# Kernel optimization log

Hardware: AMD Instinct MI355X
Metric: run time of the kernel (lower is better)

## Reference

```python
import jax, jax.numpy as jnp
import numpy as np

N, IN_FEATURES, OUT_FEATURES = 131072, 128, 512


def setup_inputs() -> dict:
    key = jax.random.key(0)
    k1, k2 = jax.random.split(key)
    x = jax.random.normal(k1, (N, IN_FEATURES), dtype=jnp.float32)
    centers = jax.random.normal(k2, (OUT_FEATURES, IN_FEATURES), dtype=jnp.float32)  # nn.init.normal_(0,1)
    log_sigmas = jnp.zeros((OUT_FEATURES,), dtype=jnp.float32)  # nn.init.constant_(0)
    return {"x": x, "centers": centers, "log_sigmas": log_sigmas}


def reference(x, centers, log_sigmas):
    # (N, out, in) expanded intermediate of the torch code; same math).
    x_sq = jnp.sum(x * x, axis=-1, keepdims=True)            # (N, 1)
    c_sq = jnp.sum(centers * centers, axis=-1)               # (out,)
    cross = x @ centers.T                                    # (N, out) GEMM
    d2 = jnp.maximum(x_sq - 2.0 * cross + c_sq[None, :], 0.0)
    distances = jnp.sqrt(d2) / jnp.exp(log_sigmas)[None, :]  # (N, out)
    # gaussian basis: phi(r) = exp(-r^2)
    return jnp.exp(-(distances * distances))
```

## Files before the change

### kernel.cpp

```cpp
#include <hip/hip_runtime.h>
#include <hip/hip_bf16.h>


typedef __attribute__((ext_vector_type(8))) short bf16x8;
typedef __attribute__((ext_vector_type(4))) float f32x4;
typedef __attribute__((ext_vector_type(4))) unsigned u32x4;

#define KDIM 128
#define ODIM 512
#define LOG2E 1.4426950408889634f

union BF8 { unsigned u[4]; bf16x8 v; u32x4 q; };

__device__ __forceinline__ unsigned pack_bf2(float a, float b) {
    unsigned ua = __builtin_bit_cast(unsigned, a);
    unsigned ub = __builtin_bit_cast(unsigned, b);
    ua += 0x7fffu + ((ua >> 16) & 1u);
    ub += 0x7fffu + ((ub >> 16) & 1u);
    return (ua >> 16) | (ub & 0xffff0000u);
}

__global__ __launch_bounds__(256) void rbf_pack_kernel(
    const float* __restrict__ centers,
    const float* __restrict__ log_sigmas,
    u32x4* __restrict__ wsfrag,
    float* __restrict__ wsis,
    float* __restrict__ wscs)
{
    const int b = blockIdx.x;
    if (b < 32) {
        int i  = b * 256 + threadIdx.x;
        int g  = i >> 8;
        int kk = (i >> 6) & 3;
        int l  = i & 63;
        int c  = g * 16 + (l & 15);
        int k0 = kk * 32 + (l >> 4) * 8;
        const f32x4* p = (const f32x4*)(centers + (size_t)c * KDIM + k0);
        f32x4 v0 = p[0], v1 = p[1];
        BF8 w;
        w.u[0] = pack_bf2(v0.x, v0.y);
        w.u[1] = pack_bf2(v0.z, v0.w);
        w.u[2] = pack_bf2(v1.x, v1.y);
        w.u[3] = pack_bf2(v1.z, v1.w);
        wsfrag[i] = w.q;
    } else {
        int c = (b - 32) * 256 + threadIdx.x;
        const f32x4* p = (const f32x4*)(centers + (size_t)c * KDIM);
        float s = 0.f;
        #pragma unroll
        for (int k = 0; k < 32; ++k) {
            f32x4 v = p[k];
            s += v.x*v.x + v.y*v.y + v.z*v.z + v.w*v.w;
        }
        float a = __expf(-2.0f * log_sigmas[c]) * LOG2E;
        wsis[c] = a;
        wscs[c] = s * a;
    }
}

__global__ __launch_bounds__(1024, 4) void rbf_main_kernel(
    const float* __restrict__ x,
    const u32x4* __restrict__ wsfrag,
    const f32x4* __restrict__ wsis4,
    const f32x4* __restrict__ wscs4,
    float* __restrict__ out)
{
    __shared__ u32x4 sF[8192];
    __shared__ float sIS[ODIM];
    __shared__ float sCS[ODIM];

    const int t  = threadIdx.x;
    const int w  = t >> 6;
    const int l  = t & 63;
    const int lr = l & 15;
    const int lk = l >> 4;

    #pragma unroll
    for (int i = 0; i < 8; ++i)
        sF[i * 1024 + t] = wsfrag[i * 1024 + t];
    if (t < 128) {
        ((f32x4*)sIS)[t] = wsis4[t];
        ((f32x4*)sCS)[t] = wscs4[t];
    }
    __syncthreads();

    const int r0 = blockIdx.x * 512 + w * 32;
    bf16x8 xf0[4], xf1[4];
    float xsq0, xsq1;
#define LOADX(XF, XS, ROWOFF)                                                  \
    {                                                                          \
        const float* xp = x + (size_t)(r0 + (ROWOFF) + lr) * KDIM + lk * 8;    \
        float s = 0.f;                                                         \
        _Pragma("unroll")                                                      \
        for (int kk = 0; kk < 4; ++kk) {                                       \
            const f32x4* p = (const f32x4*)(xp + kk * 32);                     \
            f32x4 v0 = p[0], v1 = p[1];                                        \
            s += v0.x*v0.x + v0.y*v0.y + v0.z*v0.z + v0.w*v0.w                 \
               + v1.x*v1.x + v1.y*v1.y + v1.z*v1.z + v1.w*v1.w;                \
            BF8 bw;                                                            \
            bw.u[0] = pack_bf2(v0.x, v0.y);                                    \
            bw.u[1] = pack_bf2(v0.z, v0.w);                                    \
            bw.u[2] = pack_bf2(v1.x, v1.y);                                    \
            bw.u[3] = pack_bf2(v1.z, v1.w);                                    \
            XF[kk] = bw.v;                                                     \
        }                                                                      \
        s += __shfl_xor(s, 16);                                                \
        s += __shfl_xor(s, 32);                                                \
        XS = s;                                                                \
    }
    LOADX(xf0, xsq0, 0)
    LOADX(xf1, xsq1, 16)
#undef LOADX

    float* orow0 = out + (size_t)(r0 + lr) * ODIM;
    float* orow1 = orow0 + (size_t)16 * ODIM;

    const bf16x8* fB = (const bf16x8*)sF + l;

    #pragma unroll 2
    for (int g = 0; g < 32; ++g) {
        f32x4 a0 = (f32x4){0.f, 0.f, 0.f, 0.f};
        f32x4 a1 = (f32x4){0.f, 0.f, 0.f, 0.f};
        #pragma unroll
        for (int kk = 0; kk < 4; ++kk) {
            bf16x8 cf = fB[(g * 4 + kk) * 64];
            a0 = __builtin_amdgcn_mfma_f32_16x16x32_bf16(cf, xf0[kk], a0, 0, 0, 0);
            a1 = __builtin_amdgcn_mfma_f32_16x16x32_bf16(cf, xf1[kk], a1, 0, 0, 0);
        }
        const int cb = g * 16 + lk * 4;
        f32x4 A4 = *(const f32x4*)&sIS[cb];
        f32x4 B4 = *(const f32x4*)&sCS[cb];
        f32x4 o0, o1;
        o0.x = exp2f(-fmaxf(fmaf(A4.x, fmaf(-2.f, a0[0], xsq0), B4.x), 0.f));
        o0.y = exp2f(-fmaxf(fmaf(A4.y, fmaf(-2.f, a0[1], xsq0), B4.y), 0.f));
        o0.z = exp2f(-fmaxf(fmaf(A4.z, fmaf(-2.f, a0[2], xsq0), B4.z), 0.f));
        o0.w = exp2f(-fmaxf(fmaf(A4.w, fmaf(-2.f, a0[3], xsq0), B4.w), 0.f));
        o1.x = exp2f(-fmaxf(fmaf(A4.x, fmaf(-2.f, a1[0], xsq1), B4.x), 0.f));
        o1.y = exp2f(-fmaxf(fmaf(A4.y, fmaf(-2.f, a1[1], xsq1), B4.y), 0.f));
        o1.z = exp2f(-fmaxf(fmaf(A4.z, fmaf(-2.f, a1[2], xsq1), B4.z), 0.f));
        o1.w = exp2f(-fmaxf(fmaf(A4.w, fmaf(-2.f, a1[3], xsq1), B4.w), 0.f));
        *(f32x4*)(orow0 + cb) = o0;
        *(f32x4*)(orow1 + cb) = o1;
    }
}

__global__ __launch_bounds__(1024, 1) void rbf_fallback_kernel(
    const float* __restrict__ x,
    const float* __restrict__ centers,
    const float* __restrict__ log_sigmas,
    float* __restrict__ out)
{
    __shared__ u32x4 sC[ODIM * 16];
    __shared__ float sIS[ODIM];
    __shared__ float sCS[ODIM];

    const int t  = threadIdx.x;
    const int w  = t >> 6;
    const int l  = t & 63;
    const int lr = l & 15;
    const int lk = l >> 4;

    #pragma unroll
    for (int i = 0; i < 8; ++i) {
        int c    = i * 1024 + t;
        int row  = c >> 4;
        int col8 = c & 15;
        const f32x4* gp = (const f32x4*)(centers + (size_t)row * KDIM + col8 * 8);
        f32x4 v0 = gp[0], v1 = gp[1];
        float s = v0.x*v0.x + v0.y*v0.y + v0.z*v0.z + v0.w*v0.w
                + v1.x*v1.x + v1.y*v1.y + v1.z*v1.z + v1.w*v1.w;
        s += __shfl_xor(s, 1); s += __shfl_xor(s, 2);
        s += __shfl_xor(s, 4); s += __shfl_xor(s, 8);
        BF8 wv;
        wv.u[0] = pack_bf2(v0.x, v0.y);
        wv.u[1] = pack_bf2(v0.z, v0.w);
        wv.u[2] = pack_bf2(v1.x, v1.y);
        wv.u[3] = pack_bf2(v1.z, v1.w);
        int byte = row * 256 + col8 * 16;
        byte ^= (row & 7) << 4;
        *(u32x4*)((char*)sC + byte) = wv.q;
        if ((t & 15) == 0) {
            float a = __expf(-2.0f * log_sigmas[row]);
            sIS[row] = a;
            sCS[row] = s * a;
        }
    }
    __syncthreads();

    const int r0 = blockIdx.x * 512 + w * 32;
    bf16x8 xf[2][4];
    float  xsq[2];
    #pragma unroll
    for (int tt = 0; tt < 2; ++tt) {
        const float* xp = x + (size_t)(r0 + tt * 16 + lr) * KDIM + lk * 8;
        float s = 0.f;
        #pragma unroll
        for (int kk = 0; kk < 4; ++kk) {
            const f32x4* p = (const f32x4*)(xp + kk * 32);
            f32x4 v0 = p[0], v1 = p[1];
            s += v0.x*v0.x + v0.y*v0.y + v0.z*v0.z + v0.w*v0.w
               + v1.x*v1.x + v1.y*v1.y + v1.z*v1.z + v1.w*v1.w;
            BF8 b;
            b.u[0] = pack_bf2(v0.x, v0.y);
            b.u[1] = pack_bf2(v0.z, v0.w);
            b.u[2] = pack_bf2(v1.x, v1.y);
            b.u[3] = pack_bf2(v1.z, v1.w);
            xf[tt][kk] = b.v;
        }
        s += __shfl_xor(s, 16);
        s += __shfl_xor(s, 32);
        xsq[tt] = s;
    }

    float* orow0 = out + (size_t)(r0 + lr) * ODIM;
    float* orow1 = out + (size_t)(r0 + 16 + lr) * ODIM;

    #pragma unroll 2
    for (int g = 0; g < 32; ++g) {
        bf16x8 af[4];
        #pragma unroll
        for (int kk = 0; kk < 4; ++kk) {
            int row  = g * 16 + lr;
            int byte = row * 256 + kk * 64 + lk * 16;
            byte ^= (row & 7) << 4;
            af[kk] = *(const bf16x8*)((const char*)sC + byte);
        }
        f32x4 a0 = (f32x4){0.f, 0.f, 0.f, 0.f};
        f32x4 a1 = (f32x4){0.f, 0.f, 0.f, 0.f};
        #pragma unroll
        for (int kk = 0; kk < 4; ++kk) {
            a0 = __builtin_amdgcn_mfma_f32_16x16x32_bf16(af[kk], xf[0][kk], a0, 0, 0, 0);
            a1 = __builtin_amdgcn_mfma_f32_16x16x32_bf16(af[kk], xf[1][kk], a1, 0, 0, 0);
        }
        const int cb = g * 16 + lk * 4;
        f32x4 A4 = *(const f32x4*)&sIS[cb];
        f32x4 B4 = *(const f32x4*)&sCS[cb];
        f32x4 o0, o1;
        o0.x = __expf(-fmaxf(fmaf(A4.x, fmaf(-2.f, a0[0], xsq[0]), B4.x), 0.f));
        o0.y = __expf(-fmaxf(fmaf(A4.y, fmaf(-2.f, a0[1], xsq[0]), B4.y), 0.f));
        o0.z = __expf(-fmaxf(fmaf(A4.z, fmaf(-2.f, a0[2], xsq[0]), B4.z), 0.f));
        o0.w = __expf(-fmaxf(fmaf(A4.w, fmaf(-2.f, a0[3], xsq[0]), B4.w), 0.f));
        o1.x = __expf(-fmaxf(fmaf(A4.x, fmaf(-2.f, a1[0], xsq[1]), B4.x), 0.f));
        o1.y = __expf(-fmaxf(fmaf(A4.y, fmaf(-2.f, a1[1], xsq[1]), B4.y), 0.f));
        o1.z = __expf(-fmaxf(fmaf(A4.z, fmaf(-2.f, a1[2], xsq[1]), B4.z), 0.f));
        o1.w = __expf(-fmaxf(fmaf(A4.w, fmaf(-2.f, a1[3], xsq[1]), B4.w), 0.f));
        *(f32x4*)(orow0 + cb) = o0;
        *(f32x4*)(orow1 + cb) = o1;
    }
}

extern "C" void kernel_launch(void* const* d_in, const int* in_sizes, int n_in,
                              void* d_out, int out_size, void* d_ws, size_t ws_size,
                              hipStream_t stream) {
    const float* x          = (const float*)d_in[0];
    const float* centers    = (const float*)d_in[1];
    const float* log_sigmas = (const float*)d_in[2];
    float* out = (float*)d_out;

    const int n_rows = in_sizes[0] / KDIM;

    const size_t WS_NEED = 128 * 1024 + 2 * 2048;
    if (ws_size >= WS_NEED) {
        u32x4* wsfrag = (u32x4*)d_ws;
        float* wsis   = (float*)((char*)d_ws + 128 * 1024);
        float* wscs   = (float*)((char*)d_ws + 128 * 1024 + 2048);
        rbf_pack_kernel<<<34, 256, 0, stream>>>(centers, log_sigmas,
                                                wsfrag, wsis, wscs);
        rbf_main_kernel<<<n_rows / 512, 1024, 0, stream>>>(
            x, wsfrag, (const f32x4*)wsis, (const f32x4*)wscs, out);
    } else {
        rbf_fallback_kernel<<<n_rows / 512, 1024, 0, stream>>>(
            x, centers, log_sigmas, out);
    }
}
```

Before: 92.19 us.

## Halve block size, give each wave 64 rows, prefetch second x half during compute

```diff
diff --git a/kernel.cpp b/kernel.cpp
--- a/kernel.cpp
+++ b/kernel.cpp
@@ -58,7 +58,7 @@
     }
 }
 
-__global__ __launch_bounds__(1024, 4) void rbf_main_kernel(
+__global__ __launch_bounds__(512, 1) void rbf_main_kernel(
     const float* __restrict__ x,
     const u32x4* __restrict__ wsfrag,
     const f32x4* __restrict__ wsis4,
@@ -76,72 +76,102 @@
     const int lk = l >> 4;
 
     #pragma unroll
-    for (int i = 0; i < 8; ++i)
-        sF[i * 1024 + t] = wsfrag[i * 1024 + t];
+    for (int i = 0; i < 16; ++i)
+        sF[i * 512 + t] = wsfrag[i * 512 + t];
     if (t < 128) {
         ((f32x4*)sIS)[t] = wsis4[t];
         ((f32x4*)sCS)[t] = wscs4[t];
     }
     __syncthreads();
 
-    const int r0 = blockIdx.x * 512 + w * 32;
-    bf16x8 xf0[4], xf1[4];
-    float xsq0, xsq1;
-#define LOADX(XF, XS, ROWOFF)                                                  \
+    const int r0 = blockIdx.x * 512 + w * 64;
+    const bf16x8* fB = (const bf16x8*)sF + l;
+
+#define XLOAD(RW, HOFF)                                                        \
     {                                                                          \
-        const float* xp = x + (size_t)(r0 + (ROWOFF) + lr) * KDIM + lk * 8;    \
-        float s = 0.f;                                                         \
+        const float* xp0 = x + (size_t)(r0 + (HOFF) + lr) * KDIM + lk * 8;     \
+        const float* xp1 = xp0 + 16 * KDIM;                                    \
         _Pragma("unroll")                                                      \
         for (int kk = 0; kk < 4; ++kk) {                                       \
-            const f32x4* p = (const f32x4*)(xp + kk * 32);                     \
-            f32x4 v0 = p[0], v1 = p[1];                                        \
-            s += v0.x*v0.x + v0.y*v0.y + v0.z*v0.z + v0.w*v0.w                 \
-               + v1.x*v1.x + v1.y*v1.y + v1.z*v1.z + v1.w*v1.w;                \
+            RW[kk * 2]     = ((const f32x4*)(xp0 + kk * 32))[0];               \
+            RW[kk * 2 + 1] = ((const f32x4*)(xp0 + kk * 32))[1];               \
+            RW[8 + kk * 2]     = ((const f32x4*)(xp1 + kk * 32))[0];           \
+            RW[8 + kk * 2 + 1] = ((const f32x4*)(xp1 + kk * 32))[1];           \
+        }                                                                      \
+    }
+
+#define XPACK(RW, XF0, XF1, XS0, XS1)                                          \
+    {                                                                          \
+        float s0 = 0.f, s1 = 0.f;                                              \
+        _Pragma("unroll")                                                      \
+        for (int kk = 0; kk < 4; ++kk) {                                       \
+            f32x4 v0 = RW[kk * 2], v1 = RW[kk * 2 + 1];                        \
+            s0 += v0.x*v0.x + v0.y*v0.y + v0.z*v0.z + v0.w*v0.w                \
+                + v1.x*v1.x + v1.y*v1.y + v1.z*v1.z + v1.w*v1.w;               \
             BF8 bw;                                                            \
             bw.u[0] = pack_bf2(v0.x, v0.y);                                    \
             bw.u[1] = pack_bf2(v0.z, v0.w);                                    \
             bw.u[2] = pack_bf2(v1.x, v1.y);                                    \
             bw.u[3] = pack_bf2(v1.z, v1.w);                                    \
-            XF[kk] = bw.v;                                                     \
+            XF0[kk] = bw.v;                                                    \
+            v0 = RW[8 + kk * 2]; v1 = RW[8 + kk * 2 + 1];                      \
+            s1 += v0.x*v0.x + v0.y*v0.y + v0.z*v0.z + v0.w*v0.w                \
+                + v1.x*v1.x + v1.y*v1.y + v1.z*v1.z + v1.w*v1.w;               \
+            bw.u[0] = pack_bf2(v0.x, v0.y);                                    \
+            bw.u[1] = pack_bf2(v0.z, v0.w);                                    \
+            bw.u[2] = pack_bf2(v1.x, v1.y);                                    \
+            bw.u[3] = pack_bf2(v1.z, v1.w);                                    \
+            XF1[kk] = bw.v;                                                    \
         }                                                                      \
-        s += __shfl_xor(s, 16);                                                \
-        s += __shfl_xor(s, 32);                                                \
-        XS = s;                                                                \
-    }
-    LOADX(xf0, xsq0, 0)
-    LOADX(xf1, xsq1, 16)
-#undef LOADX
-
-    float* orow0 = out + (size_t)(r0 + lr) * ODIM;
-    float* orow1 = orow0 + (size_t)16 * ODIM;
-
-    const bf16x8* fB = (const bf16x8*)sF + l;
-
-    #pragma unroll 2
-    for (int g = 0; g < 32; ++g) {
-        f32x4 a0 = (f32x4){0.f, 0.f, 0.f, 0.f};
-        f32x4 a1 = (f32x4){0.f, 0.f, 0.f, 0.f};
-        #pragma unroll
-        for (int kk = 0; kk < 4; ++kk) {
-            bf16x8 cf = fB[(g * 4 + kk) * 64];
-            a0 = __builtin_amdgcn_mfma_f32_16x16x32_bf16(cf, xf0[kk], a0, 0, 0, 0);
-            a1 = __builtin_amdgcn_mfma_f32_16x16x32_bf16(cf, xf1[kk], a1, 0, 0, 0);
-        }
-        const int cb = g * 16 + lk * 4;
-        f32x4 A4 = *(const f32x4*)&sIS[cb];
-        f32x4 B4 = *(const f32x4*)&sCS[cb];
-        f32x4 o0, o1;
-        o0.x = exp2f(-fmaxf(fmaf(A4.x, fmaf(-2.f, a0[0], xsq0), B4.x), 0.f));
-        o0.y = exp2f(-fmaxf(fmaf(A4.y, fmaf(-2.f, a0[1], xsq0), B4.y), 0.f));
-        o0.z = exp2f(-fmaxf(fmaf(A4.z, fmaf(-2.f, a0[2], xsq0), B4.z), 0.f));
-        o0.w = exp2f(-fmaxf(fmaf(A4.w, fmaf(-2.f, a0[3], xsq0), B4.w), 0.f));
-        o1.x = exp2f(-fmaxf(fmaf(A4.x, fmaf(-2.f, a1[0], xsq1), B4.x), 0.f));
-        o1.y = exp2f(-fmaxf(fmaf(A4.y, fmaf(-2.f, a1[1], xsq1), B4.y), 0.f));
-        o1.z = exp2f(-fmaxf(fmaf(A4.z, fmaf(-2.f, a1[2], xsq1), B4.z), 0.f));
-        o1.w = exp2f(-fmaxf(fmaf(A4.w, fmaf(-2.f, a1[3], xsq1), B4.w), 0.f));
-        *(f32x4*)(orow0 + cb) = o0;
-        *(f32x4*)(orow1 + cb) = o1;
-    }
+        s0 += __shfl_xor(s0, 16); s0 += __shfl_xor(s0, 32);                    \
+        s1 += __shfl_xor(s1, 16); s1 += __shfl_xor(s1, 32);                    \
+        XS0 = s0; XS1 = s1;                                                    \
+    }
+
+#define HALF(XF0, XF1, XS0, XS1, HOFF)                                         \
+    {                                                                          \
+        float* orow0 = out + (size_t)(r0 + (HOFF) + lr) * ODIM;                \
+        float* orow1 = orow0 + (size_t)16 * ODIM;                              \
+        _Pragma("unroll 2")                                                    \
+        for (int g = 0; g < 32; ++g) {                                         \
+            f32x4 a0 = (f32x4){0.f, 0.f, 0.f, 0.f};                            \
+            f32x4 a1 = (f32x4){0.f, 0.f, 0.f, 0.f};                            \
+            _Pragma("unroll")                                                  \
+            for (int kk = 0; kk < 4; ++kk) {                                   \
+                bf16x8 cf = fB[(g * 4 + kk) * 64];                             \
+                a0 = __builtin_amdgcn_mfma_f32_16x16x32_bf16(cf, XF0[kk], a0, 0, 0, 0); \
+                a1 = __builtin_amdgcn_mfma_f32_16x16x32_bf16(cf, XF1[kk], a1, 0, 0, 0); \
+            }                                                                  \
+            const int cb = g * 16 + lk * 4;                                    \
+            f32x4 A4 = *(const f32x4*)&sIS[cb];                                \
+            f32x4 B4 = *(const f32x4*)&sCS[cb];                                \
+            f32x4 o0, o1;                                                      \
+            o0.x = exp2f(-fmaxf(fmaf(A4.x, fmaf(-2.f, a0[0], XS0), B4.x), 0.f)); \
+            o0.y = exp2f(-fmaxf(fmaf(A4.y, fmaf(-2.f, a0[1], XS0), B4.y), 0.f)); \
+            o0.z = exp2f(-fmaxf(fmaf(A4.z, fmaf(-2.f, a0[2], XS0), B4.z), 0.f)); \
+            o0.w = exp2f(-fmaxf(fmaf(A4.w, fmaf(-2.f, a0[3], XS0), B4.w), 0.f)); \
+            o1.x = exp2f(-fmaxf(fmaf(A4.x, fmaf(-2.f, a1[0], XS1), B4.x), 0.f)); \
+            o1.y = exp2f(-fmaxf(fmaf(A4.y, fmaf(-2.f, a1[1], XS1), B4.y), 0.f)); \
+            o1.z = exp2f(-fmaxf(fmaf(A4.z, fmaf(-2.f, a1[2], XS1), B4.z), 0.f)); \
+            o1.w = exp2f(-fmaxf(fmaf(A4.w, fmaf(-2.f, a1[3], XS1), B4.w), 0.f)); \
+            *(f32x4*)(orow0 + cb) = o0;                                        \
+            *(f32x4*)(orow1 + cb) = o1;                                        \
+        }                                                                      \
+    }
+
+    f32x4 raw[16];
+    bf16x8 xfA0[4], xfA1[4], xfB0[4], xfB1[4];
+    float sA0, sA1, sB0, sB1;
+
+    XLOAD(raw, 0)
+    XPACK(raw, xfA0, xfA1, sA0, sA1)
+    XLOAD(raw, 32)
+    HALF(xfA0, xfA1, sA0, sA1, 0)
+    XPACK(raw, xfB0, xfB1, sB0, sB1)
+    HALF(xfB0, xfB1, sB0, sB1, 32)
+#undef HALF
+#undef XPACK
+#undef XLOAD
 }
 
 __global__ __launch_bounds__(1024, 1) void rbf_fallback_kernel(
@@ -266,7 +296,7 @@
         float* wscs   = (float*)((char*)d_ws + 128 * 1024 + 2048);
         rbf_pack_kernel<<<34, 256, 0, stream>>>(centers, log_sigmas,
                                                 wsfrag, wsis, wscs);
-        rbf_main_kernel<<<n_rows / 512, 1024, 0, stream>>>(
+        rbf_main_kernel<<<n_rows / 512, 512, 0, stream>>>(
             x, wsfrag, (const f32x4*)wsis, (const f32x4*)wscs, out);
     } else {
         rbf_fallback_kernel<<<n_rows / 512, 1024, 0, stream>>>(
```

Result: faster. 89.52 us (-2.9%).
